# Performance work log

Measured on AMD Instinct MI355X. Metric: run time of the kernel, lower is better.

The kernel has to match this reference:

```python
import jax, jax.numpy as jnp
import numpy as np

D_MODEL = 512
N_HEADS = 8
D_K = D_MODEL // N_HEADS
B, T = 8, 2048


def setup_inputs() -> dict:
    key = jax.random.key(0)
    ks = jax.random.split(key, 8)
    s = 0.02
    return {
        "x": jax.random.normal(ks[0], (B, T, D_MODEL), dtype=jnp.float32),
        "mask": jnp.zeros((B, T), dtype=bool),
        "ln_w": jnp.ones((D_MODEL,), dtype=jnp.float32),
        "ln_b": jnp.zeros((D_MODEL,), dtype=jnp.float32),
        "w_qkv": jax.random.normal(ks[1], (D_MODEL, 3 * D_MODEL), dtype=jnp.float32) * s,
        "b_qkv": jnp.zeros((3 * D_MODEL,), dtype=jnp.float32),
        "w_o": jax.random.normal(ks[2], (D_MODEL, D_MODEL), dtype=jnp.float32) * s,
        "b_o": jnp.zeros((D_MODEL,), dtype=jnp.float32),
    }


def _rope(q, k):
    # q, k: (B, H, T, d_k); standard GPT-NeoX-style rotary embedding
    t = q.shape[2]
    inv_freq = 1.0 / (10000.0 ** (jnp.arange(0, D_K, 2, dtype=jnp.float32) / D_K))
    ang = jnp.arange(t, dtype=jnp.float32)[:, None] * inv_freq[None, :]  # (T, d_k/2)
    cos = jnp.concatenate([jnp.cos(ang), jnp.cos(ang)], axis=-1)  # (T, d_k)
    sin = jnp.concatenate([jnp.sin(ang), jnp.sin(ang)], axis=-1)

    def rot_half(x):
        x1, x2 = x[..., : D_K // 2], x[..., D_K // 2 :]
        return jnp.concatenate([-x2, x1], axis=-1)

    q = q * cos + rot_half(q) * sin
    k = k * cos + rot_half(k) * sin
    return q, k


def reference(x, mask, ln_w, ln_b, w_qkv, b_qkv, w_o, b_o):
    Bv, Tv, Dv = x.shape
    # LayerNorm
    mu = jnp.mean(x, axis=-1, keepdims=True)
    var = jnp.mean(jnp.square(x - mu), axis=-1, keepdims=True)
    h = (x - mu) / jnp.sqrt(var + 1e-5) * ln_w + ln_b
    # QKV projection
    qkv = h @ w_qkv + b_qkv  # (B, T, 3D)
    qkv = qkv.reshape(Bv, Tv, 3, N_HEADS, D_K).transpose(2, 0, 3, 1, 4)
    q, k, v = qkv[0], qkv[1], qkv[2]  # each (B, H, T, d_k)
    q, k = _rope(q, k)
    scale = jnp.sqrt(jnp.asarray(D_K, dtype=x.dtype))
    attn = jnp.einsum("bhqd,bhkd->bhqk", q, k) / scale
    attn = jnp.where(mask[:, None, None, :], -jnp.inf, attn)
    attn = jax.nn.softmax(attn, axis=-1)
    out = jnp.einsum("bhqk,bhkd->bhqd", attn, v)  # (B, H, T, d_k)
    out = out.transpose(0, 2, 1, 3).reshape(Bv, Tv, Dv)
    return out @ w_o + b_o
```

## Files before the change

### kernel.cpp

```cpp
#include <hip/hip_runtime.h>
#include <hip/hip_bf16.h>

#define TT 2048

typedef __attribute__((ext_vector_type(8))) short bf16x8;
typedef __attribute__((ext_vector_type(4))) float f32x4;
typedef __attribute__((ext_vector_type(16))) float f32x16;
typedef __attribute__((ext_vector_type(2))) int i32x2;

__device__ __forceinline__ short f2b(float f) {
  union { float f; unsigned u; } a; a.f = f;
  unsigned r = a.u + 0x7fffu + ((a.u >> 16) & 1u);
  return (short)(r >> 16);
}
__device__ __forceinline__ float b2f(short s) {
  union { unsigned u; float f; } a; a.u = ((unsigned)(unsigned short)s) << 16;
  return a.f;
}
__device__ __forceinline__ unsigned cvtpk(float lo, float hi) {
  unsigned r;
  asm("v_cvt_pk_bf16_f32 %0, %1, %2" : "=v"(r) : "v"(lo), "v"(hi));
  return r;
}
__device__ __forceinline__ float max3f(float a, float b, float c) {
  float d;
  asm("v_max3_f32 %0, %1, %2, %3" : "=v"(d) : "v"(a), "v"(b), "v"(c));
  return d;
}
__device__ __forceinline__ float ex2(float x) {
#if __has_builtin(__builtin_amdgcn_exp2f)
  return __builtin_amdgcn_exp2f(x);
#else
  return exp2f(x);
#endif
}
__device__ __forceinline__ void gll16(const void* g, void* l) {
  __builtin_amdgcn_global_load_lds(
      (const __attribute__((address_space(1))) unsigned int*)g,
      (__attribute__((address_space(3))) unsigned int*)l, 16, 0, 0);
}
__device__ __forceinline__ void swap_halves(unsigned &a, unsigned &b, bool hi) {
#if __has_builtin(__builtin_amdgcn_permlane32_swap)
  i32x2 r = __builtin_amdgcn_permlane32_swap((int)a, (int)b, false, false);
  a = (unsigned)r[0]; b = (unsigned)r[1];
#else
  unsigned as = (unsigned)__shfl_xor((int)a, 32);
  unsigned bs = (unsigned)__shfl_xor((int)b, 32);
  unsigned na = hi ? bs : a;
  unsigned nb = hi ? b : as;
  a = na; b = nb;
#endif
}

__device__ __forceinline__ void p_to_frags(const f32x16 p, bool hi, bf16x8* f0, bf16x8* f1) {
  unsigned A[4][2];
#pragma unroll
  for (int u = 0; u < 4; ++u)
#pragma unroll
    for (int c = 0; c < 2; ++c)
      A[u][c] = cvtpk(p[4 * u + 2 * c], p[4 * u + 2 * c + 1]);
  swap_halves(A[0][0], A[1][0], hi);
  swap_halves(A[0][1], A[1][1], hi);
  swap_halves(A[2][0], A[3][0], hi);
  swap_halves(A[2][1], A[3][1], hi);
  union { unsigned u[4]; bf16x8 v; } r0, r1;
  r0.u[0] = A[0][0]; r0.u[1] = A[0][1]; r0.u[2] = A[1][0]; r0.u[3] = A[1][1];
  r1.u[0] = A[2][0]; r1.u[1] = A[2][1]; r1.u[2] = A[3][0]; r1.u[3] = A[3][1];
  *f0 = r0.v; *f1 = r1.v;
}

__device__ __forceinline__ bf16x8 lds16(const short* base, int row, int cb) {
  return *reinterpret_cast<const bf16x8*>(
      reinterpret_cast<const char*>(base) + row * 128 + (cb ^ ((row & 7) << 4)));
}

__global__ __launch_bounds__(256) void tcast_kernel(const float* __restrict__ src,
                                                    short* __restrict__ dst, int N) {
  __shared__ float t[64][65];
  const int n0 = blockIdx.x * 64, k0 = blockIdx.y * 64;
  const int c = threadIdx.x & 63, r4 = threadIdx.x >> 6;
#pragma unroll
  for (int i = 0; i < 16; ++i) {
    const int r = i * 4 + r4;
    t[r][c] = src[(size_t)(k0 + r) * N + n0 + c];
  }
  __syncthreads();
#pragma unroll
  for (int i = 0; i < 16; ++i) {
    const int r = i * 4 + r4;
    dst[(size_t)(n0 + r) * 512 + k0 + c] = f2b(t[c][r]);
  }
}

__global__ __launch_bounds__(256) void ropetab_kernel(float2* __restrict__ tab) {
  const int idx = blockIdx.x * 256 + threadIdx.x;
  const int i = idx & 31, t = idx >> 5;
  const float inv_freq = __expf(-(float)i * (9.210340371976184f / 32.0f));
  float sv, cv;
  sincosf((float)t * inv_freq, &sv, &cv);
  tab[idx] = make_float2(cv, sv);
}

__global__ __launch_bounds__(256) void ln_kernel(const float* __restrict__ x,
                                                 const float* __restrict__ w,
                                                 const float* __restrict__ b,
                                                 short* __restrict__ h) {
  const int row = blockIdx.x;
  const int tid = threadIdx.x;
  const float2 v = *reinterpret_cast<const float2*>(x + (size_t)row * 512 + tid * 2);
  float s = v.x + v.y;
  float sq = v.x * v.x + v.y * v.y;
  for (int off = 1; off < 64; off <<= 1) { s += __shfl_xor(s, off); sq += __shfl_xor(sq, off); }
  __shared__ float red[8];
  const int wv = tid >> 6;
  if ((tid & 63) == 0) { red[wv] = s; red[wv + 4] = sq; }
  __syncthreads();
  s = red[0] + red[1] + red[2] + red[3];
  sq = red[4] + red[5] + red[6] + red[7];
  const float mu = s * (1.0f / 512.0f);
  const float var = sq * (1.0f / 512.0f) - mu * mu;
  const float inv = rsqrtf(var + 1e-5f);
  const float2 wv2 = *reinterpret_cast<const float2*>(w + tid * 2);
  const float2 bv2 = *reinterpret_cast<const float2*>(b + tid * 2);
  const float h0 = (v.x - mu) * inv * wv2.x + bv2.x;
  const float h1 = (v.y - mu) * inv * wv2.y + bv2.y;
  unsigned u = (unsigned)(unsigned short)f2b(h0) | ((unsigned)(unsigned short)f2b(h1) << 16);
  *reinterpret_cast<unsigned*>(h + (size_t)row * 512 + tid * 2) = u;
}

template <int EPI>
__global__ __launch_bounds__(256) void gemm128_kernel(const short* __restrict__ A,
                                                      const short* __restrict__ Bt,
                                                      const float* __restrict__ bias,
                                                      const float2* __restrict__ tab,
                                                      void* __restrict__ o0,
                                                      void* __restrict__ o1,
                                                      void* __restrict__ o2) {
  __shared__ short As[128 * 64];
  __shared__ short Bs[128 * 64];
  const int tid = threadIdx.x;
  const int lane = tid & 63, wave = tid >> 6;
  const int lr = lane & 15, lg = lane >> 4;
  const int wm = wave >> 1, wn = wave & 1;
  const int m0 = blockIdx.x * 128, n0 = blockIdx.y * 128;

  const int swz_col = ((lane & 7) ^ ((lane >> 3) & 7)) * 8;
  const short* Ag = A + (size_t)(m0 + wave * 32 + (lane >> 3)) * 512 + swz_col;
  const short* Bg = Bt + (size_t)(n0 + wave * 32 + (lane >> 3)) * 512 + swz_col;
  short* AsW = &As[(wave * 32) * 64];
  short* BsW = &Bs[(wave * 32) * 64];

  f32x4 acc[4][4] = {};

  for (int k0 = 0; k0 < 512; k0 += 64) {
#pragma unroll
    for (int i = 0; i < 4; ++i) {
      gll16(Ag + (size_t)i * 8 * 512 + k0, AsW + i * 8 * 64);
      gll16(Bg + (size_t)i * 8 * 512 + k0, BsW + i * 8 * 64);
    }
    __syncthreads();
#pragma unroll
    for (int ks = 0; ks < 2; ++ks) {
      bf16x8 af[4], bfr[4];
#pragma unroll
      for (int m = 0; m < 4; ++m)
        af[m] = lds16(As, wm * 64 + m * 16 + lr, ks * 64 + lg * 16);
#pragma unroll
      for (int n = 0; n < 4; ++n)
        bfr[n] = lds16(Bs, wn * 64 + n * 16 + lr, ks * 64 + lg * 16);
#pragma unroll
      for (int m = 0; m < 4; ++m)
#pragma unroll
        for (int n = 0; n < 4; ++n)
          acc[m][n] = __builtin_amdgcn_mfma_f32_16x16x32_bf16(af[m], bfr[n], acc[m][n], 0, 0, 0);
    }
    __syncthreads();
  }

  if (EPI == 0) {
    const int base = n0 + wn * 64;
    const int which = base >> 9;
    const int hh = (base & 511) >> 6;
    short* qp = (short*)o0; short* kp = (short*)o1; short* vtp = (short*)o2;
    const float b0 = bias[base + lr], b1 = bias[base + 16 + lr];
    const float b2 = bias[base + 32 + lr], b3 = bias[base + 48 + lr];
    const float QS = 0.125f * 1.4426950408889634f;
#pragma unroll
    for (int m = 0; m < 4; ++m) {
      const int rowb = m0 + wm * 64 + m * 16 + lg * 4;
#pragma unroll
      for (int j = 0; j < 4; ++j) {
        const int t = (rowb + j) & 2047;
        const int bh = ((rowb + j) >> 11) * 8 + hh;
        float v0 = acc[m][0][j] + b0;
        float v1 = acc[m][1][j] + b1;
        float v2 = acc[m][2][j] + b2;
        float v3 = acc[m][3][j] + b3;
        if (which < 2) {
          const float2 cs0 = tab[t * 32 + lr];
          const float2 cs1 = tab[t * 32 + 16 + lr];
          float r0 = v0 * cs0.x - v2 * cs0.y;
          float r2 = v2 * cs0.x + v0 * cs0.y;
          float r1 = v1 * cs1.x - v3 * cs1.y;
          float r3 = v3 * cs1.x + v1 * cs1.y;
          if (which == 0) { r0 *= QS; r1 *= QS; r2 *= QS; r3 *= QS; }
          short* dst = (which == 0 ? qp : kp) + ((size_t)bh * TT + t) * 64;
          dst[lr] = f2b(r0); dst[16 + lr] = f2b(r1);
          dst[32 + lr] = f2b(r2); dst[48 + lr] = f2b(r3);
        } else {
          short* vb = vtp + (size_t)bh * 64 * TT + t;
          vb[(size_t)lr * TT] = f2b(v0);
          vb[(size_t)(16 + lr) * TT] = f2b(v1);
          vb[(size_t)(32 + lr) * TT] = f2b(v2);
          vb[(size_t)(48 + lr) * TT] = f2b(v3);
        }
      }
    }
  } else {
#pragma unroll
    for (int m = 0; m < 4; ++m)
#pragma unroll
      for (int n = 0; n < 4; ++n)
#pragma unroll
        for (int j = 0; j < 4; ++j) {
          const int row = m0 + wm * 64 + m * 16 + lg * 4 + j;
          const int col = n0 + wn * 64 + n * 16 + lr;
          ((float*)o0)[(size_t)row * 512 + col] = acc[m][n][j] + bias[col];
        }
  }
}

__global__ __launch_bounds__(512) void attn_kernel(const short* __restrict__ q,
                                                   const short* __restrict__ k,
                                                   const short* __restrict__ vt,
                                                   const unsigned char* __restrict__ mask,
                                                   short* __restrict__ o) {
  __shared__ short Ks[2][64 * 64];
  __shared__ short Vs[2][64 * 64];
  __shared__ float psc[8][32];
  const int tid = threadIdx.x;
  const int lane = tid & 63, wave = tid >> 6;
  const int l31 = lane & 31, g = lane >> 5;
  const bool hi = (g != 0);
  const int nb = (blockIdx.x & 7) * 64 + (blockIdx.x >> 3);
  const int bh = nb >> 3, qt = nb & 7;
  const int bb = bh >> 3, hh = bh & 7;
  const int q0 = qt * 256 + wave * 32;
  const size_t bhT = (size_t)bh * TT;
  const unsigned char* maskb = mask + (size_t)bb * TT;

  bf16x8 qf[4];
#pragma unroll
  for (int ds = 0; ds < 4; ++ds)
    qf[ds] = *reinterpret_cast<const bf16x8*>(q + (bhT + q0 + l31) * 64 + ds * 16 + g * 8);

  f32x16 oa0 = {}, oa1 = {};
  float m_run = 0.0f, l_run = 0.0f;

  const int swz_col = ((lane & 7) ^ ((lane >> 3) & 7)) * 8;
  const int r0 = wave * 8;
  const short* kg0 = k + (bhT + r0 + (lane >> 3)) * 64 + swz_col;
  const short* vg0 = vt + ((size_t)bh * 64 + r0 + (lane >> 3)) * TT + swz_col;

  gll16(kg0, &Ks[0][r0 * 64]);
  gll16(vg0, &Vs[0][r0 * 64]);
  __syncthreads();

  unsigned mq = 0;
  for (int kt = 0; kt < TT / 64; ++kt) {
    const int cur = kt & 1;
    if (kt < TT / 64 - 1) {
      const int nxt = cur ^ 1;
      gll16(kg0 + (size_t)(kt + 1) * 64 * 64, &Ks[nxt][r0 * 64]);
      gll16(vg0 + (size_t)(kt + 1) * 64, &Vs[nxt][r0 * 64]);
    }
    if ((kt & 3) == 0) mq = *(const unsigned*)(maskb + kt * 64 + lane * 4);

    const short* Kc = Ks[cur];
    const short* Vc = Vs[cur];

    f32x16 s0 = {}, s1 = {};
    __builtin_amdgcn_s_setprio(1);
#pragma unroll
    for (int ds = 0; ds < 4; ++ds) {
      const int cb = ds * 32 + g * 16;
      const bf16x8 ka0 = lds16(Kc, l31, cb);
      const bf16x8 ka1 = lds16(Kc, 32 + l31, cb);
      s0 = __builtin_amdgcn_mfma_f32_32x32x16_bf16(ka0, qf[ds], s0, 0, 0, 0);
      s1 = __builtin_amdgcn_mfma_f32_32x32x16_bf16(ka1, qf[ds], s1, 0, 0, 0);
    }
    __builtin_amdgcn_s_setprio(0);

    if (__any((int)(mq != 0))) {
#pragma unroll
      for (int r = 0; r < 16; ++r) {
        const int kk = (r & 3) + 8 * (r >> 2) + 4 * g;
        if (maskb[kt * 64 + kk]) s0[r] += -1e30f;
        if (maskb[kt * 64 + 32 + kk]) s1[r] += -1e30f;
      }
    }

    float b8[8];
#pragma unroll
    for (int i = 0; i < 8; ++i) b8[i] = max3f(s0[i], s0[i + 8], s1[i]);
    float c4[4];
#pragma unroll
    for (int i = 0; i < 4; ++i) c4[i] = fmaxf(s1[8 + i], s1[12 + i]);
    const float d0 = max3f(b8[0], b8[1], b8[2]);
    const float d1 = max3f(b8[3], b8[4], b8[5]);
    const float d2 = max3f(b8[6], b8[7], c4[0]);
    const float d3 = max3f(c4[1], c4[2], c4[3]);
    const float mx = fmaxf(max3f(d0, d1, d2), d3);
    const float pmax = fmaxf(mx, __shfl_xor(mx, 32));

    if (kt == 0) {
      m_run = pmax;
    } else if (!__all((int)(pmax - m_run <= 8.0f))) {
      const float nm = fmaxf(m_run, pmax);
      const float sc = ex2(m_run - nm);
      m_run = nm;
      l_run *= sc;
      if (lane < 32) psc[wave][l31] = sc;
      asm volatile("s_waitcnt lgkmcnt(0)" ::: "memory");
#pragma unroll
      for (int r = 0; r < 16; ++r) {
        const float s = psc[wave][(r & 3) + 8 * (r >> 2) + 4 * g];
        oa0[r] *= s; oa1[r] *= s;
      }
    }

#pragma unroll
    for (int i = 0; i < 16; ++i) { s0[i] = ex2(s0[i] - m_run); s1[i] = ex2(s1[i] - m_run); }

    float a8[8];
#pragma unroll
    for (int i = 0; i < 8; ++i) a8[i] = (s0[i] + s0[i + 8]) + (s1[i] + s1[i + 8]);
    const float e0 = (a8[0] + a8[1]) + (a8[2] + a8[3]);
    const float e1 = (a8[4] + a8[5]) + (a8[6] + a8[7]);
    const float rsum = e0 + e1;
    l_run += rsum + __shfl_xor(rsum, 32);

    bf16x8 pa[4];
    p_to_frags(s0, hi, &pa[0], &pa[1]);
    p_to_frags(s1, hi, &pa[2], &pa[3]);

    __builtin_amdgcn_s_setprio(1);
#pragma unroll
    for (int ks = 0; ks < 4; ++ks) {
      const int cb = ks * 32 + g * 16;
      const bf16x8 vb0 = lds16(Vc, l31, cb);
      const bf16x8 vb1 = lds16(Vc, 32 + l31, cb);
      oa0 = __builtin_amdgcn_mfma_f32_32x32x16_bf16(pa[ks], vb0, oa0, 0, 0, 0);
      oa1 = __builtin_amdgcn_mfma_f32_32x32x16_bf16(pa[ks], vb1, oa1, 0, 0, 0);
    }
    __builtin_amdgcn_s_setprio(0);

    __syncthreads();
  }

  const float linv = 1.0f / l_run;
#pragma unroll
  for (int r = 0; r < 16; ++r) {
    const int qr = (r & 3) + 8 * (r >> 2) + 4 * g;
    const float lv = __shfl(linv, (lane & 32) | qr, 64);
    const int trow = q0 + qr;
    const size_t orow = ((size_t)bb * TT + trow) * 512 + hh * 64 + l31;
    o[orow]      = f2b(oa0[r] * lv);
    o[orow + 32] = f2b(oa1[r] * lv);
  }
}

extern "C" void kernel_launch(void* const* d_in, const int* in_sizes, int n_in,
                              void* d_out, int out_size, void* d_ws, size_t ws_size,
                              hipStream_t stream) {
  (void)in_sizes; (void)n_in; (void)out_size; (void)ws_size;
  const float* x = (const float*)d_in[0];
  const unsigned char* mask = (const unsigned char*)d_in[1];
  const float* ln_w = (const float*)d_in[2];
  const float* ln_b = (const float*)d_in[3];
  const float* w_qkv = (const float*)d_in[4];
  const float* b_qkv = (const float*)d_in[5];
  const float* w_o = (const float*)d_in[6];
  const float* b_o = (const float*)d_in[7];
  float* out = (float*)d_out;

  char* ws = (char*)d_ws;
  short* h_buf = (short*)(ws);
  short* wqkvT = (short*)(ws + 16777216);
  short* woT   = (short*)(ws + 18350080);
  short* q_ws  = (short*)(ws + 18874368);
  short* k_ws  = (short*)(ws + 35651584);
  short* vt_ws = (short*)(ws + 52428800);
  float2* tab  = (float2*)(ws + 69206016);

  hipLaunchKernelGGL(tcast_kernel, dim3(24, 8), dim3(256), 0, stream, w_qkv, wqkvT, 1536);
  hipLaunchKernelGGL(tcast_kernel, dim3(8, 8), dim3(256), 0, stream, w_o, woT, 512);
  hipLaunchKernelGGL(ropetab_kernel, dim3(256), dim3(256), 0, stream, tab);
  hipLaunchKernelGGL(ln_kernel, dim3(16384), dim3(256), 0, stream, x, ln_w, ln_b, h_buf);
  hipLaunchKernelGGL((gemm128_kernel<0>), dim3(128, 12), dim3(256), 0, stream,
                     h_buf, wqkvT, b_qkv, tab, (void*)q_ws, (void*)k_ws, (void*)vt_ws);
  hipLaunchKernelGGL(attn_kernel, dim3(512), dim3(512), 0, stream,
                     q_ws, k_ws, vt_ws, mask, h_buf);
  hipLaunchKernelGGL((gemm128_kernel<1>), dim3(128, 4), dim3(256), 0, stream,
                     h_buf, woT, b_o, tab, (void*)out, nullptr, nullptr);
}
```

Before: 179.6 us.

## Software-pipeline attention QK with softmax-PV, triple-buffer K/V, merge prep kernels

The attention kernel now runs 4 waves per block with 128 query rows and 1024 blocks. K/V tiles are triple-buffered, and QK^T for tile kt is issued before the softmax and PV of tile kt-1, so MFMA work can overlap the exponent and max math. The mask check is hoisted to a single per-block OR over the whole row. Weight transposes and the rope table are merged into one prep kernel to save launches. The cost is more live registers from two sets of score accumulators, plus extra LDS for the third buffer.

```diff
diff --git a/kernel.cpp b/kernel.cpp
--- a/kernel.cpp
+++ b/kernel.cpp
@@ -74,31 +74,37 @@
       reinterpret_cast<const char*>(base) + row * 128 + (cb ^ ((row & 7) << 4)));
 }
 
-__global__ __launch_bounds__(256) void tcast_kernel(const float* __restrict__ src,
-                                                    short* __restrict__ dst, int N) {
+__global__ __launch_bounds__(256) void prep_kernel(const float* __restrict__ w_qkv,
+                                                   short* __restrict__ wqkvT,
+                                                   const float* __restrict__ w_o,
+                                                   short* __restrict__ woT,
+                                                   float2* __restrict__ tab) {
   __shared__ float t[64][65];
-  const int n0 = blockIdx.x * 64, k0 = blockIdx.y * 64;
-  const int c = threadIdx.x & 63, r4 = threadIdx.x >> 6;
-#pragma unroll
-  for (int i = 0; i < 16; ++i) {
-    const int r = i * 4 + r4;
-    t[r][c] = src[(size_t)(k0 + r) * N + n0 + c];
+  const int id = blockIdx.x;
+  if (id < 256) {
+    const float* src; short* dst; int N, n0, k0;
+    if (id < 192) { src = w_qkv; dst = wqkvT; N = 1536; n0 = (id % 24) * 64; k0 = (id / 24) * 64; }
+    else { const int i2 = id - 192; src = w_o; dst = woT; N = 512; n0 = (i2 & 7) * 64; k0 = (i2 >> 3) * 64; }
+    const int c = threadIdx.x & 63, r4 = threadIdx.x >> 6;
+#pragma unroll
+    for (int i = 0; i < 16; ++i) {
+      const int r = i * 4 + r4;
+      t[r][c] = src[(size_t)(k0 + r) * N + n0 + c];
+    }
+    __syncthreads();
+#pragma unroll
+    for (int i = 0; i < 16; ++i) {
+      const int r = i * 4 + r4;
+      dst[(size_t)(n0 + r) * 512 + k0 + c] = f2b(t[c][r]);
+    }
+  } else {
+    const int idx = (id - 256) * 256 + threadIdx.x;
+    const int i = idx & 31, tt = idx >> 5;
+    const float inv_freq = __expf(-(float)i * (9.210340371976184f / 32.0f));
+    float sv, cv;
+    sincosf((float)tt * inv_freq, &sv, &cv);
+    tab[idx] = make_float2(cv, sv);
   }
-  __syncthreads();
-#pragma unroll
-  for (int i = 0; i < 16; ++i) {
-    const int r = i * 4 + r4;
-    dst[(size_t)(n0 + r) * 512 + k0 + c] = f2b(t[c][r]);
-  }
-}
-
-__global__ __launch_bounds__(256) void ropetab_kernel(float2* __restrict__ tab) {
-  const int idx = blockIdx.x * 256 + threadIdx.x;
-  const int i = idx & 31, t = idx >> 5;
-  const float inv_freq = __expf(-(float)i * (9.210340371976184f / 32.0f));
-  float sv, cv;
-  sincosf((float)t * inv_freq, &sv, &cv);
-  tab[idx] = make_float2(cv, sv);
 }
 
 __global__ __launch_bounds__(256) void ln_kernel(const float* __restrict__ x,
@@ -230,25 +236,31 @@
   }
 }
 
-__global__ __launch_bounds__(512) void attn_kernel(const short* __restrict__ q,
+__global__ __launch_bounds__(256) void attn_kernel(const short* __restrict__ q,
                                                    const short* __restrict__ k,
                                                    const short* __restrict__ vt,
                                                    const unsigned char* __restrict__ mask,
                                                    short* __restrict__ o) {
-  __shared__ short Ks[2][64 * 64];
-  __shared__ short Vs[2][64 * 64];
-  __shared__ float psc[8][32];
+  __shared__ short Ks[3][64 * 64];
+  __shared__ short Vs[3][64 * 64];
+  __shared__ float psc[4][32];
   const int tid = threadIdx.x;
   const int lane = tid & 63, wave = tid >> 6;
   const int l31 = lane & 31, g = lane >> 5;
   const bool hi = (g != 0);
-  const int nb = (blockIdx.x & 7) * 64 + (blockIdx.x >> 3);
-  const int bh = nb >> 3, qt = nb & 7;
+  const int nb = (blockIdx.x & 7) * 128 + (blockIdx.x >> 3);
+  const int bh = nb >> 4, qt = nb & 15;
   const int bb = bh >> 3, hh = bh & 7;
-  const int q0 = qt * 256 + wave * 32;
+  const int q0 = qt * 128 + wave * 32;
   const size_t bhT = (size_t)bh * TT;
   const unsigned char* maskb = mask + (size_t)bb * TT;
 
+  unsigned mor = 0;
+  const unsigned* mw = (const unsigned*)maskb;
+#pragma unroll
+  for (int i = 0; i < 8; ++i) mor |= mw[lane + 64 * i];
+  const bool masked = __any((int)(mor != 0));
+
   bf16x8 qf[4];
 #pragma unroll
   for (int ds = 0; ds < 4; ++ds)
@@ -258,48 +270,41 @@
   float m_run = 0.0f, l_run = 0.0f;
 
   const int swz_col = ((lane & 7) ^ ((lane >> 3) & 7)) * 8;
-  const int r0 = wave * 8;
+  const int r0 = wave * 16;
   const short* kg0 = k + (bhT + r0 + (lane >> 3)) * 64 + swz_col;
   const short* vg0 = vt + ((size_t)bh * 64 + r0 + (lane >> 3)) * TT + swz_col;
 
-  gll16(kg0, &Ks[0][r0 * 64]);
-  gll16(vg0, &Vs[0][r0 * 64]);
-  __syncthreads();
-
-  unsigned mq = 0;
-  for (int kt = 0; kt < TT / 64; ++kt) {
-    const int cur = kt & 1;
-    if (kt < TT / 64 - 1) {
-      const int nxt = cur ^ 1;
-      gll16(kg0 + (size_t)(kt + 1) * 64 * 64, &Ks[nxt][r0 * 64]);
-      gll16(vg0 + (size_t)(kt + 1) * 64, &Vs[nxt][r0 * 64]);
-    }
-    if ((kt & 3) == 0) mq = *(const unsigned*)(maskb + kt * 64 + lane * 4);
-
-    const short* Kc = Ks[cur];
-    const short* Vc = Vs[cur];
-
-    f32x16 s0 = {}, s1 = {};
+  auto stage = [&](int kt, int buf) {
+    gll16(kg0 + (size_t)kt * 4096,          &Ks[buf][r0 * 64]);
+    gll16(kg0 + (size_t)kt * 4096 + 8 * 64, &Ks[buf][(r0 + 8) * 64]);
+    gll16(vg0 + (size_t)kt * 64,            &Vs[buf][r0 * 64]);
+    gll16(vg0 + (size_t)kt * 64 + 8 * TT,   &Vs[buf][(r0 + 8) * 64]);
+  };
+
+  auto qk = [&](const short* Kc, f32x16& t0, f32x16& t1) {
+    f32x16 a = {}, b = {};
     __builtin_amdgcn_s_setprio(1);
 #pragma unroll
     for (int ds = 0; ds < 4; ++ds) {
       const int cb = ds * 32 + g * 16;
       const bf16x8 ka0 = lds16(Kc, l31, cb);
       const bf16x8 ka1 = lds16(Kc, 32 + l31, cb);
-      s0 = __builtin_amdgcn_mfma_f32_32x32x16_bf16(ka0, qf[ds], s0, 0, 0, 0);
-      s1 = __builtin_amdgcn_mfma_f32_32x32x16_bf16(ka1, qf[ds], s1, 0, 0, 0);
+      a = __builtin_amdgcn_mfma_f32_32x32x16_bf16(ka0, qf[ds], a, 0, 0, 0);
+      b = __builtin_amdgcn_mfma_f32_32x32x16_bf16(ka1, qf[ds], b, 0, 0, 0);
     }
     __builtin_amdgcn_s_setprio(0);
-
-    if (__any((int)(mq != 0))) {
+    t0 = a; t1 = b;
+  };
+
+  auto smpv = [&](int j, f32x16& s0, f32x16& s1, const short* Vc) {
+    if (masked) {
 #pragma unroll
       for (int r = 0; r < 16; ++r) {
         const int kk = (r & 3) + 8 * (r >> 2) + 4 * g;
-        if (maskb[kt * 64 + kk]) s0[r] += -1e30f;
-        if (maskb[kt * 64 + 32 + kk]) s1[r] += -1e30f;
+        if (maskb[j * 64 + kk]) s0[r] += -1e30f;
+        if (maskb[j * 64 + 32 + kk]) s1[r] += -1e30f;
       }
     }
-
     float b8[8];
 #pragma unroll
     for (int i = 0; i < 8; ++i) b8[i] = max3f(s0[i], s0[i + 8], s1[i]);
@@ -313,7 +318,7 @@
     const float mx = fmaxf(max3f(d0, d1, d2), d3);
     const float pmax = fmaxf(mx, __shfl_xor(mx, 32));
 
-    if (kt == 0) {
+    if (j == 0) {
       m_run = pmax;
     } else if (!__all((int)(pmax - m_run <= 8.0f))) {
       const float nm = fmaxf(m_run, pmax);
@@ -322,6 +327,7 @@
       l_run *= sc;
       if (lane < 32) psc[wave][l31] = sc;
       asm volatile("s_waitcnt lgkmcnt(0)" ::: "memory");
+      __builtin_amdgcn_sched_barrier(0);
 #pragma unroll
       for (int r = 0; r < 16; ++r) {
         const float s = psc[wave][(r & 3) + 8 * (r >> 2) + 4 * g];
@@ -340,23 +346,43 @@
     const float rsum = e0 + e1;
     l_run += rsum + __shfl_xor(rsum, 32);
 
-    bf16x8 pa[4];
-    p_to_frags(s0, hi, &pa[0], &pa[1]);
-    p_to_frags(s1, hi, &pa[2], &pa[3]);
-
+    bf16x8 f0, f1;
     __builtin_amdgcn_s_setprio(1);
-#pragma unroll
-    for (int ks = 0; ks < 4; ++ks) {
-      const int cb = ks * 32 + g * 16;
-      const bf16x8 vb0 = lds16(Vc, l31, cb);
-      const bf16x8 vb1 = lds16(Vc, 32 + l31, cb);
-      oa0 = __builtin_amdgcn_mfma_f32_32x32x16_bf16(pa[ks], vb0, oa0, 0, 0, 0);
-      oa1 = __builtin_amdgcn_mfma_f32_32x32x16_bf16(pa[ks], vb1, oa1, 0, 0, 0);
+    p_to_frags(s0, hi, &f0, &f1);
+    {
+      const int cb0 = 0 * 32 + g * 16, cb1 = 1 * 32 + g * 16;
+      oa0 = __builtin_amdgcn_mfma_f32_32x32x16_bf16(f0, lds16(Vc, l31, cb0), oa0, 0, 0, 0);
+      oa1 = __builtin_amdgcn_mfma_f32_32x32x16_bf16(f0, lds16(Vc, 32 + l31, cb0), oa1, 0, 0, 0);
+      oa0 = __builtin_amdgcn_mfma_f32_32x32x16_bf16(f1, lds16(Vc, l31, cb1), oa0, 0, 0, 0);
+      oa1 = __builtin_amdgcn_mfma_f32_32x32x16_bf16(f1, lds16(Vc, 32 + l31, cb1), oa1, 0, 0, 0);
+    }
+    p_to_frags(s1, hi, &f0, &f1);
+    {
+      const int cb2 = 2 * 32 + g * 16, cb3 = 3 * 32 + g * 16;
+      oa0 = __builtin_amdgcn_mfma_f32_32x32x16_bf16(f0, lds16(Vc, l31, cb2), oa0, 0, 0, 0);
+      oa1 = __builtin_amdgcn_mfma_f32_32x32x16_bf16(f0, lds16(Vc, 32 + l31, cb2), oa1, 0, 0, 0);
+      oa0 = __builtin_amdgcn_mfma_f32_32x32x16_bf16(f1, lds16(Vc, l31, cb3), oa0, 0, 0, 0);
+      oa1 = __builtin_amdgcn_mfma_f32_32x32x16_bf16(f1, lds16(Vc, 32 + l31, cb3), oa1, 0, 0, 0);
     }
     __builtin_amdgcn_s_setprio(0);
-
+  };
+
+  f32x16 sA0, sA1, sB0, sB1;
+
+  stage(0, 0);
+  __syncthreads();
+  stage(1, 1);
+  qk(Ks[0], sA0, sA1);
+  __syncthreads();
+
+  for (int kt = 1; kt < TT / 64; ++kt) {
+    const int bi = kt % 3, pv = (kt - 1) % 3, nx = (kt + 1) % 3;
+    if (kt + 1 < TT / 64) stage(kt + 1, nx);
+    if (kt & 1) { qk(Ks[bi], sB0, sB1); smpv(kt - 1, sA0, sA1, Vs[pv]); }
+    else        { qk(Ks[bi], sA0, sA1); smpv(kt - 1, sB0, sB1, Vs[pv]); }
     __syncthreads();
   }
+  smpv(TT / 64 - 1, sB0, sB1, Vs[(TT / 64 - 1) % 3]);
 
   const float linv = 1.0f / l_run;
 #pragma unroll
@@ -393,13 +419,12 @@
   short* vt_ws = (short*)(ws + 52428800);
   float2* tab  = (float2*)(ws + 69206016);
 
-  hipLaunchKernelGGL(tcast_kernel, dim3(24, 8), dim3(256), 0, stream, w_qkv, wqkvT, 1536);
-  hipLaunchKernelGGL(tcast_kernel, dim3(8, 8), dim3(256), 0, stream, w_o, woT, 512);
-  hipLaunchKernelGGL(ropetab_kernel, dim3(256), dim3(256), 0, stream, tab);
+  hipLaunchKernelGGL(prep_kernel, dim3(512), dim3(256), 0, stream,
+                     w_qkv, wqkvT, w_o, woT, tab);
   hipLaunchKernelGGL(ln_kernel, dim3(16384), dim3(256), 0, stream, x, ln_w, ln_b, h_buf);
   hipLaunchKernelGGL((gemm128_kernel<0>), dim3(128, 12), dim3(256), 0, stream,
                      h_buf, wqkvT, b_qkv, tab, (void*)q_ws, (void*)k_ws, (void*)vt_ws);
-  hipLaunchKernelGGL(attn_kernel, dim3(512), dim3(512), 0, stream,
+  hipLaunchKernelGGL(attn_kernel, dim3(1024), dim3(256), 0, stream,
                      q_ws, k_ws, vt_ws, mask, h_buf);
   hipLaunchKernelGGL((gemm128_kernel<1>), dim3(128, 4), dim3(256), 0, stream,
                      h_buf, woT, b_o, tab, (void*)out, nullptr, nullptr);
```

After: 315.8 us. +75.9%, slower.
